# Kernel optimization log

Measured on AMD Instinct MI355X. Metric: run time of the kernel, lower is better.

The kernel has to match this reference:

```python
import jax, jax.numpy as jnp
import numpy as np

N = 50000      # nodes
E = 800000     # edges per relation
R = 2          # relations
L = 2          # conv layers
D = 128        # hidden / input channels
G = 64         # graphs in batch
C = 8          # num_classes


def setup_inputs() -> dict:
    key = jax.random.key(0)
    ks = jax.random.split(key, 6)
    x = jax.random.normal(ks[0], (N, D), dtype=jnp.float32)
    W = jax.random.normal(ks[1], (L, R, D, D), dtype=jnp.float32) * 0.05
    b = jnp.zeros((L, R, D), dtype=jnp.float32)
    lin_w = jax.random.normal(ks[2], (D, C), dtype=jnp.float32) * 0.05
    lin_b = jnp.zeros((C,), dtype=jnp.float32)
    edge_index = jax.random.randint(ks[3], (R, 2, E), 0, N, dtype=jnp.int32)
    batch = jnp.sort(jax.random.randint(ks[4], (N,), 0, G, dtype=jnp.int32))
    return {"x": x, "W": W, "b": b, "lin_w": lin_w, "lin_b": lin_b,
            "edge_index": edge_index, "batch": batch}


def _gcn_conv(x, src, dst, inv_sqrt_deg, W_r, b_r):
    """PyG GCNConv: symmetric-normalized aggregation with self loops.
    out[i] = sum_{j->i} d_i^-1/2 d_j^-1/2 (x_j W) + d_i^-1 (x_i W) + b
    where d includes the self loop (in-degree + 1)."""
    xw = x @ W_r                                   # [N, D]
    norm = inv_sqrt_deg[src] * inv_sqrt_deg[dst]   # [E]
    agg = jax.ops.segment_sum(xw[src] * norm[:, None], dst, num_segments=N)
    agg = agg + xw * (inv_sqrt_deg * inv_sqrt_deg)[:, None]  # self-loop msg
    return agg + b_r


def reference(x, W, b, lin_w, lin_b, edge_index, batch):
    # Pre-compute per-relation symmetric normalization (same for all layers).
    inv_sqrt_degs = []
    for r in range(R):
        dst = edge_index[r, 1]
        deg = jax.ops.segment_sum(jnp.ones((E,), x.dtype), dst, num_segments=N) + 1.0
        inv_sqrt_degs.append(jax.lax.rsqrt(deg))

    h = x
    for l in range(L):
        out = jnp.zeros((N, D), x.dtype)
        for r in range(R):  # HeteroConv aggr='sum' over relations
            out = out + _gcn_conv(h, edge_index[r, 0], edge_index[r, 1],
                                  inv_sqrt_degs[r], W[l, r], b[l, r])
        h = jax.nn.relu(out) if l < L - 1 else out

    # global_mean_pool over batch ids
    counts = jax.ops.segment_sum(jnp.ones((N,), x.dtype), batch, num_segments=G)
    sums = jax.ops.segment_sum(h, batch, num_segments=G)
    pooled = sums / jnp.maximum(counts, 1.0)[:, None]   # [G, D]
    # dropout(p=0.5) is identity in eval mode; final Linear
    return pooled @ lin_w + lin_b                        # [G, C]
```

## Files before the change

### kernel.cpp

```cpp
#include <hip/hip_runtime.h>
#include <math.h>

#define NN 50000
#define EE 800000
#define RR 2
#define LL 2
#define DD 128
#define GG 64
#define CCLS 8
#define NBUK 196
#define BCAP 6144
#define BCI2 14080

typedef unsigned int uint;
typedef unsigned short ushort;
typedef short bf16x8 __attribute__((ext_vector_type(8)));
typedef float f32x4 __attribute__((ext_vector_type(4)));
typedef float f32x2 __attribute__((ext_vector_type(2)));

#define OFF_H1    ((size_t)0)
#define OFF_WBT   ((size_t)12800000)
#define OFF_ISD   ((size_t)12931072)
#define OFF_RP    ((size_t)13331072)
#define OFF_CI    ((size_t)13732480)
#define OFF_ZERO  ((size_t)24771200)
#define OFF_BD    ((size_t)24805824)
#define OFF_XW    ((size_t)24805824)
#define ZO_GCUR 0
#define ZO_SUM  1600
#define ZO_CNT  34368
#define ZERO_BYTES 34624

static __device__ __forceinline__ ushort f2b(float f) {
  uint u = __float_as_uint(f);
  uint r = (u + 0x7fffu + ((u >> 16) & 1u)) >> 16;
  return (ushort)r;
}
static __device__ __forceinline__ float blo(uint u) { return __uint_as_float(u << 16); }
static __device__ __forceinline__ float bhi(uint u) { return __uint_as_float(u & 0xffff0000u); }

__global__ __launch_bounds__(256) void k_wprep(const float* __restrict__ W,
                                               ushort* __restrict__ WT) {
  int idx = blockIdx.x * 256 + threadIdx.x;
  int lr = idx >> 14;
  int rem = idx & 16383;
  int n = rem >> 7, k = rem & 127;
  WT[lr * 16384 + n * 128 + k] = f2b(W[lr * 16384 + k * 128 + n]);
}

__global__ __launch_bounds__(256) void k_part(const int* __restrict__ EI,
                                              int* __restrict__ gcur,
                                              uint* __restrict__ bdata) {
  __shared__ int hist[256];
  __shared__ int sbase[256];
  __shared__ int gbase[256];
  __shared__ int lcur[256];
  __shared__ uint stage[4096];
  __shared__ unsigned char bstage[4096];
  const int r = blockIdx.y;
  const int t = threadIdx.x;
  const int e0 = blockIdx.x * 4096;
  const int cnt = min(4096, EE - e0);
  hist[t] = 0;
  lcur[t] = 0;
  __syncthreads();

  int src[16], dst[16];
  bool val[4];
#pragma unroll
  for (int j = 0; j < 4; ++j) {
    int i4 = (j * 256 + t) * 4;
    val[j] = (i4 < cnt);
    if (val[j]) {
      int4 s4 = *(const int4*)(EI + (size_t)r * 2 * EE + e0 + i4);
      int4 d4 = *(const int4*)(EI + (size_t)r * 2 * EE + EE + e0 + i4);
      src[j * 4 + 0] = s4.x; src[j * 4 + 1] = s4.y; src[j * 4 + 2] = s4.z; src[j * 4 + 3] = s4.w;
      dst[j * 4 + 0] = d4.x; dst[j * 4 + 1] = d4.y; dst[j * 4 + 2] = d4.z; dst[j * 4 + 3] = d4.w;
#pragma unroll
      for (int i = 0; i < 4; ++i) atomicAdd(&hist[dst[j * 4 + i] >> 8], 1);
    }
  }
  __syncthreads();
  int hv = hist[t];
  if (t < NBUK && hv > 0)
    gbase[t] = atomicAdd(&gcur[r * NBUK + t], hv);
  else
    gbase[t] = 0;
  sbase[t] = hv;
  __syncthreads();
  for (int off = 1; off < 256; off <<= 1) {
    int u = (t >= off) ? sbase[t - off] : 0;
    __syncthreads();
    sbase[t] += u;
    __syncthreads();
  }
  int incl = sbase[t];
  hist[t] = incl - hv;
  __syncthreads();
#pragma unroll
  for (int j = 0; j < 4; ++j) {
    if (val[j]) {
#pragma unroll
      for (int i = 0; i < 4; ++i) {
        int d = dst[j * 4 + i];
        int b = d >> 8;
        int p = atomicAdd(&lcur[b], 1);
        int pos = hist[b] + p;
        stage[pos] = ((uint)src[j * 4 + i] << 8) | (uint)(d & 255);
        bstage[pos] = (unsigned char)b;
      }
    }
  }
  __syncthreads();
  for (int s = t; s < cnt; s += 256) {
    int b = (int)bstage[s];
    bdata[(size_t)(r * NBUK + b) * BCAP + gbase[b] + (s - hist[b])] = stage[s];
  }
}

__global__ __launch_bounds__(256) void k_csr(const uint* __restrict__ bdata,
                                             const int* __restrict__ gcur,
                                             float* __restrict__ isd,
                                             int* __restrict__ rps,
                                             int* __restrict__ rpc,
                                             int* __restrict__ ci) {
  __shared__ int lcnt0[256], lcnt1[256], lrp[256], lex[256], lend0[256];
  __shared__ int lcurA[256], lcurB[256];
  __shared__ int cstage[BCI2];
  __shared__ int shtot;
  const int b = blockIdx.x;
  const int t = threadIdx.x;
  const int cnt0 = gcur[b];
  const int cnt1 = gcur[NBUK + b];
  const uint* bd0 = bdata + (size_t)b * BCAP;
  const uint* bd1 = bdata + (size_t)(NBUK + b) * BCAP;
  lcnt0[t] = 0; lcnt1[t] = 0; lcurA[t] = 0; lcurB[t] = 0;
  __syncthreads();
  for (int s = t; s < cnt0; s += 256) atomicAdd(&lcnt0[bd0[s] & 255u], 1);
  for (int s = t; s < cnt1; s += 256) atomicAdd(&lcnt1[bd1[s] & 255u], 1);
  __syncthreads();
  const int deg0 = lcnt0[t];
  const int deg1 = lcnt1[t];
  const int node = b * 256 + t;
  const int valid = (node < NN) ? 1 : 0;
  const int nreal = deg0 + deg1 + 2;
  const int ng = valid ? ((nreal + 7) >> 3) : 0;
  const int sz = ng << 3;
  const int end0 = deg0 + 1;
  lrp[t] = sz;
  __syncthreads();
  for (int off = 1; off < 256; off <<= 1) {
    int u = (t >= off) ? lrp[t - off] : 0;
    __syncthreads();
    lrp[t] += u;
    __syncthreads();
  }
  const int incl = lrp[t];
  if (t == 255) shtot = incl;
  const int ex = incl - sz;
  lex[t] = ex;
  lend0[t] = end0;
  __syncthreads();
  const int btot = shtot;
  if (t < 32) cstage[btot + t] = NN;
  rps[node] = b * BCI2 + ex;
  rpc[node] = valid ? (ng | (end0 << 16)) : 0;
  if (valid) {
    isd[node] = rsqrtf((float)(deg0 + 1));
    isd[NN + node] = rsqrtf((float)(deg1 + 1));
    cstage[ex + deg0] = node;
    cstage[ex + end0 + deg1] = (NN + 1) + node;
    for (int p = end0 + deg1 + 1; p < sz; ++p) cstage[ex + p] = NN;
  }
  for (int s = t; s < cnt0; s += 256) {
    uint pr = bd0[s];
    int j = (int)(pr & 255u);
    int p = atomicAdd(&lcurA[j], 1);
    cstage[lex[j] + p] = (int)(pr >> 8);
  }
  for (int s = t; s < cnt1; s += 256) {
    uint pr = bd1[s];
    int j = (int)(pr & 255u);
    int p = atomicAdd(&lcurB[j], 1);
    cstage[lex[j] + lend0[j] + p] = (int)(pr >> 8) + (NN + 1);
  }
  __syncthreads();
  const int on = btot + 32;
  int* co = ci + (size_t)b * BCI2;
  for (int s = t; s < on; s += 256) co[s] = cstage[s];
}

#define AL_S 72
#define WT_S 136
template <int IN_BF16>
__global__ __launch_bounds__(256) void k_gemm(const void* __restrict__ Xv,
                                              const ushort* __restrict__ WTg,
                                              const float* __restrict__ isd,
                                              uint* __restrict__ Y) {
  __shared__ ushort WTl[128 * WT_S];
  __shared__ ushort Al[128 * AL_S];
  const int r = blockIdx.y;
  const int m0b = blockIdx.x * 128;
  const int t = threadIdx.x;
  const int w = t >> 6, L = t & 63, q = L >> 4, ln = L & 15;
  uint* Yr = Y + (size_t)r * (NN + 1) * 32;
  const ushort* WTr = WTg + (size_t)r * 16384;

#pragma unroll
  for (int i = 0; i < 8; ++i) {
    int g = t + i * 256;
    int n = g >> 4, k0 = (g & 15) * 8;
    *(uint4*)(&WTl[n * WT_S + k0]) = *(const uint4*)(WTr + n * 128 + k0);
  }

  f32x4 acc[2][8];
#pragma unroll
  for (int mt = 0; mt < 2; ++mt)
#pragma unroll
    for (int nt = 0; nt < 8; ++nt) {
      acc[mt][nt][0] = 0.f; acc[mt][nt][1] = 0.f;
      acc[mt][nt][2] = 0.f; acc[mt][nt][3] = 0.f;
    }

  for (int hh = 0; hh < 2; ++hh) {
    __syncthreads();
    {
      int row = t >> 1, ch = t & 1;
      int gm = m0b + row;
      ushort* dst = &Al[row * AL_S + ch * 32];
      if (gm < NN) {
        if (IN_BF16) {
          const uint4* xp = (const uint4*)((const ushort*)Xv + (size_t)gm * 128 + hh * 64 + ch * 32);
#pragma unroll
          for (int j = 0; j < 4; ++j) ((uint4*)dst)[j] = xp[j];
        } else {
          const float4* xp = (const float4*)((const float*)Xv + (size_t)gm * 128 + hh * 64 + ch * 32);
          ushort tmp[32];
#pragma unroll
          for (int j = 0; j < 8; ++j) {
            float4 v = xp[j];
            tmp[j * 4 + 0] = f2b(v.x); tmp[j * 4 + 1] = f2b(v.y);
            tmp[j * 4 + 2] = f2b(v.z); tmp[j * 4 + 3] = f2b(v.w);
          }
#pragma unroll
          for (int j = 0; j < 4; ++j) ((uint4*)dst)[j] = ((uint4*)tmp)[j];
        }
      } else {
        uint4 z = make_uint4(0, 0, 0, 0);
#pragma unroll
        for (int j = 0; j < 4; ++j) ((uint4*)dst)[j] = z;
      }
    }
    __syncthreads();
#pragma unroll
    for (int kk = 0; kk < 2; ++kk) {
      bf16x8 b0 = *(const bf16x8*)(&Al[(w * 32 + ln) * AL_S + kk * 32 + q * 8]);
      bf16x8 b1 = *(const bf16x8*)(&Al[(w * 32 + 16 + ln) * AL_S + kk * 32 + q * 8]);
#pragma unroll
      for (int nt = 0; nt < 8; ++nt) {
        bf16x8 a = *(const bf16x8*)(&WTl[(nt * 16 + ln) * WT_S + hh * 64 + kk * 32 + q * 8]);
        acc[0][nt] = __builtin_amdgcn_mfma_f32_16x16x32_bf16(a, b0, acc[0][nt], 0, 0, 0);
        acc[1][nt] = __builtin_amdgcn_mfma_f32_16x16x32_bf16(a, b1, acc[1][nt], 0, 0, 0);
      }
    }
  }
#pragma unroll
  for (int mt = 0; mt < 2; ++mt) {
    int m = m0b + w * 32 + mt * 16 + ln;
    if (m <= NN) {
      float sc = (m < NN) ? isd[r * NN + m] : 0.f;
      uint* yp = Yr + (size_t)m * 32;
#pragma unroll
      for (int nt = 0; nt < 8; ++nt) {
        f32x4 v = acc[mt][nt];
        uint u = __builtin_amdgcn_cvt_pk_fp8_f32(v[0] * sc, v[1] * sc, 0u, false);
        u = __builtin_amdgcn_cvt_pk_fp8_f32(v[2] * sc, v[3] * sc, u, true);
        yp[nt * 4 + q] = u;
      }
    }
  }
}

__global__ __launch_bounds__(256, 6) void k_agg(const char* __restrict__ xw,
                                                const int* __restrict__ rps,
                                                const int* __restrict__ rpc,
                                                const int* __restrict__ ci,
                                                const float* __restrict__ isd,
                                                const float* __restrict__ bias,
                                                uint* __restrict__ hout, int relu_flag) {
  const int w = threadIdx.x >> 6;
  const int lane = threadIdx.x & 63;
  const int g = lane >> 3, c = lane & 7;
  const int node = blockIdx.x * 4 + w;
  const size_t cb = (size_t)c * 16;

  const int meta = rpc[node];
  const int ng = meta & 0xffff;
  const int end0 = (meta >> 16) & 0xffff;
  const int lim = ng << 3;
  const int* ce = ci + rps[node];
  const float di0 = isd[node < NN ? node : 0];
  const float di1 = isd[NN + (node < NN ? node : 0)];

  int ip = g;
  int s0 = ce[ip]; s0 = (ip < lim) ? s0 : NN; ip += 8;
  uint4 d0 = *(const uint4*)(xw + (((size_t)(uint)s0 << 7) + cb));
  int s1 = ce[ip]; s1 = (ip < lim) ? s1 : NN; ip += 8;
  uint4 d1 = *(const uint4*)(xw + (((size_t)(uint)s1 << 7) + cb));
  int s2 = ce[ip]; s2 = (ip < lim) ? s2 : NN; ip += 8;
  uint4 d2 = *(const uint4*)(xw + (((size_t)(uint)s2 << 7) + cb));

  f32x2 acc[8];
#pragma unroll
  for (int j = 0; j < 8; ++j) { acc[j][0] = 0.f; acc[j][1] = 0.f; }

  int slotc = g;
  for (int q = 0; q < ng; ++q) {
    int s3 = ce[ip]; s3 = (ip < lim) ? s3 : NN; ip += 8;
    uint4 d3 = *(const uint4*)(xw + (((size_t)(uint)s3 << 7) + cb));
    const float sc = (slotc < end0) ? di0 : di1;
    slotc += 8;
    f32x2 sc2; sc2[0] = sc; sc2[1] = sc;
    f32x2 v;
    v = __builtin_amdgcn_cvt_pk_f32_fp8(d0.x, false); acc[0] += v * sc2;
    v = __builtin_amdgcn_cvt_pk_f32_fp8(d0.x, true);  acc[1] += v * sc2;
    v = __builtin_amdgcn_cvt_pk_f32_fp8(d0.y, false); acc[2] += v * sc2;
    v = __builtin_amdgcn_cvt_pk_f32_fp8(d0.y, true);  acc[3] += v * sc2;
    v = __builtin_amdgcn_cvt_pk_f32_fp8(d0.z, false); acc[4] += v * sc2;
    v = __builtin_amdgcn_cvt_pk_f32_fp8(d0.z, true);  acc[5] += v * sc2;
    v = __builtin_amdgcn_cvt_pk_f32_fp8(d0.w, false); acc[6] += v * sc2;
    v = __builtin_amdgcn_cvt_pk_f32_fp8(d0.w, true);  acc[7] += v * sc2;
    d0 = d1; d1 = d2; d2 = d3;
  }

#pragma unroll
  for (int mask = 8; mask <= 32; mask <<= 1) {
#pragma unroll
    for (int j = 0; j < 8; ++j) {
      f32x2 o;
      o[0] = __shfl_xor(acc[j][0], mask);
      o[1] = __shfl_xor(acc[j][1], mask);
      acc[j] += o;
    }
  }

  if (g == 0 && node < NN) {
    const float4* p0 = (const float4*)(bias + c * 16);
    const float4* p1 = (const float4*)(bias + DD + c * 16);
    float o[16];
#pragma unroll
    for (int j = 0; j < 4; ++j) {
      float4 a = p0[j], bq = p1[j];
      o[4 * j + 0] = acc[2 * j][0] + a.x + bq.x;
      o[4 * j + 1] = acc[2 * j][1] + a.y + bq.y;
      o[4 * j + 2] = acc[2 * j + 1][0] + a.z + bq.z;
      o[4 * j + 3] = acc[2 * j + 1][1] + a.w + bq.w;
    }
    if (relu_flag) {
#pragma unroll
      for (int j = 0; j < 16; ++j) o[j] = fmaxf(o[j], 0.f);
    }
    uint pk[8];
#pragma unroll
    for (int j = 0; j < 8; ++j)
      pk[j] = (uint)f2b(o[2 * j]) | ((uint)f2b(o[2 * j + 1]) << 16);
    uint4* dst = (uint4*)(hout + (size_t)node * 64) + c * 2;
    dst[0] = make_uint4(pk[0], pk[1], pk[2], pk[3]);
    dst[1] = make_uint4(pk[4], pk[5], pk[6], pk[7]);
  }
}

#define PCHUNK 32
__global__ __launch_bounds__(64) void k_pool(const uint* __restrict__ h,
                                             const int* __restrict__ batch,
                                             float* __restrict__ sums,
                                             int* __restrict__ counts) {
  int lane = threadIdx.x;
  int n0 = blockIdx.x * PCHUNK;
  int n1 = n0 + PCHUNK;
  if (n1 > NN) n1 = NN;
  if (n0 >= NN) return;
  float aLo = 0.f, aHi = 0.f;
  int cnt = 0;
  int g = batch[n0];
  uint u = h[(size_t)n0 * 64 + lane];
  for (int n = n0; n < n1; ++n) {
    uint unext = 0;
    int gnext = g;
    if (n + 1 < n1) {
      unext = h[(size_t)(n + 1) * 64 + lane];
      gnext = batch[n + 1];
    }
    aLo += blo(u);
    aHi += bhi(u);
    cnt++;
    if (n + 1 < n1 && gnext != g) {
      atomicAdd(&sums[g * DD + lane * 2], aLo);
      atomicAdd(&sums[g * DD + lane * 2 + 1], aHi);
      if (lane == 0) atomicAdd(&counts[g], cnt);
      aLo = 0.f; aHi = 0.f; cnt = 0;
      g = gnext;
    }
    u = unext;
  }
  atomicAdd(&sums[g * DD + lane * 2], aLo);
  atomicAdd(&sums[g * DD + lane * 2 + 1], aHi);
  if (lane == 0) atomicAdd(&counts[g], cnt);
}

__global__ __launch_bounds__(512) void k_final(const float* __restrict__ sums,
                                               const int* __restrict__ counts,
                                               const float* __restrict__ lin_w,
                                               const float* __restrict__ lin_b,
                                               float* __restrict__ out) {
  int t = threadIdx.x;
  int g = t >> 3, co = t & 7;
  float cnt = (float)counts[g];
  if (cnt < 1.f) cnt = 1.f;
  float inv = 1.f / cnt;
  float v = lin_b[co];
  for (int d = 0; d < DD; ++d) v += (sums[g * DD + d] * inv) * lin_w[d * CCLS + co];
  out[t] = v;
}

extern "C" void kernel_launch(void* const* d_in, const int* in_sizes, int n_in,
                              void* d_out, int out_size, void* d_ws, size_t ws_size,
                              hipStream_t stream) {
  (void)in_sizes; (void)n_in; (void)out_size; (void)ws_size;
  const float* x     = (const float*)d_in[0];
  const float* W     = (const float*)d_in[1];
  const float* b     = (const float*)d_in[2];
  const float* lin_w = (const float*)d_in[3];
  const float* lin_b = (const float*)d_in[4];
  const int*   EI    = (const int*)d_in[5];
  const int*   batch = (const int*)d_in[6];
  float* out = (float*)d_out;

  char* ws = (char*)d_ws;
  uint*   h1    = (uint*)(ws + OFF_H1);
  ushort* WbfT  = (ushort*)(ws + OFF_WBT);
  float*  isd   = (float*)(ws + OFF_ISD);
  int*    rps   = (int*)(ws + OFF_RP);
  int*    rpc   = rps + NBUK * 256;
  int*    ci    = (int*)(ws + OFF_CI);
  uint*   bdata = (uint*)(ws + OFF_BD);
  uint*   xw    = (uint*)(ws + OFF_XW);
  char*   zb    = ws + OFF_ZERO;
  int*    gcur  = (int*)(zb + ZO_GCUR);
  float*  sums  = (float*)(zb + ZO_SUM);
  int*    counts= (int*)(zb + ZO_CNT);

  (void)hipMemsetAsync(zb, 0, ZERO_BYTES, stream);

  k_wprep<<<256, 256, 0, stream>>>(W, WbfT);
  k_part<<<dim3((EE + 4095) / 4096, RR), 256, 0, stream>>>(EI, gcur, bdata);
  k_csr<<<NBUK, 256, 0, stream>>>(bdata, gcur, isd, rps, rpc, ci);

  for (int l = 0; l < LL; ++l) {
    const ushort* WTl_g = WbfT + (size_t)l * RR * DD * DD;
    if (l == 0)
      k_gemm<0><<<dim3((NN + 127) / 128, RR), 256, 0, stream>>>((const void*)x, WTl_g, isd, xw);
    else
      k_gemm<1><<<dim3((NN + 127) / 128, RR), 256, 0, stream>>>((const void*)h1, WTl_g, isd, xw);
    k_agg<<<(NBUK * 256) / 4, 256, 0, stream>>>((const char*)xw, rps, rpc, ci, isd,
                                                b + (size_t)l * RR * DD, h1,
                                                (l < LL - 1) ? 1 : 0);
  }
  k_pool<<<(NN + PCHUNK - 1) / PCHUNK, 64, 0, stream>>>(h1, batch, sums, counts);
  k_final<<<1, GG * CCLS, 0, stream>>>(sums, counts, lin_w, lin_b, out);
}
```

Measured before the change: 272.7 us.

## Split aggregation into column slices with 16 edge slots per node

The aggregation kernel now handles two nodes per wavefront with 16 edge slots each. Each lane loads 16 bytes of a 32-byte column slice, and four blocks cover the four slices of the same node group. CSR padding changes to multiples of 16 so more neighbor gathers are in flight per node. The deep three-stage prefetch becomes a single-stage one, and occupancy bounds are raised. The costs are that the CSR edge lists are re-read once per slice, low-degree nodes carry more padding, and a wave's two nodes both loop to the larger group count.

```diff
diff --git a/kernel.cpp b/kernel.cpp
--- a/kernel.cpp
+++ b/kernel.cpp
@@ -144,8 +144,8 @@
   const int node = b * 256 + t;
   const int valid = (node < NN) ? 1 : 0;
   const int nreal = deg0 + deg1 + 2;
-  const int ng = valid ? ((nreal + 7) >> 3) : 0;
-  const int sz = ng << 3;
+  const int ng = valid ? ((nreal + 15) >> 4) : 0;
+  const int sz = ng << 4;
   const int end0 = deg0 + 1;
   lrp[t] = sz;
   __syncthreads();
@@ -281,7 +281,7 @@
   }
 }
 
-__global__ __launch_bounds__(256, 6) void k_agg(const char* __restrict__ xw,
+__global__ __launch_bounds__(256, 8) void k_agg(const char* __restrict__ xw,
                                                 const int* __restrict__ rps,
                                                 const int* __restrict__ rpc,
                                                 const int* __restrict__ ci,
@@ -290,36 +290,44 @@
                                                 uint* __restrict__ hout, int relu_flag) {
   const int w = threadIdx.x >> 6;
   const int lane = threadIdx.x & 63;
-  const int g = lane >> 3, c = lane & 7;
-  const int node = blockIdx.x * 4 + w;
-  const size_t cb = (size_t)c * 16;
+  const int sub = lane >> 5;
+  const int slot = (lane >> 1) & 15;
+  const int half = lane & 1;
+  const int slice = blockIdx.x & 3;
+  const int grp = blockIdx.x >> 2;
+  const int node = grp * 8 + w * 2 + sub;
+  const int nsafe = (node < NN) ? node : 0;
 
   const int meta = rpc[node];
   const int ng = meta & 0xffff;
   const int end0 = (meta >> 16) & 0xffff;
-  const int lim = ng << 3;
+  const int lim = ng << 4;
   const int* ce = ci + rps[node];
-  const float di0 = isd[node < NN ? node : 0];
-  const float di1 = isd[NN + (node < NN ? node : 0)];
-
-  int ip = g;
-  int s0 = ce[ip]; s0 = (ip < lim) ? s0 : NN; ip += 8;
-  uint4 d0 = *(const uint4*)(xw + (((size_t)(uint)s0 << 7) + cb));
-  int s1 = ce[ip]; s1 = (ip < lim) ? s1 : NN; ip += 8;
-  uint4 d1 = *(const uint4*)(xw + (((size_t)(uint)s1 << 7) + cb));
-  int s2 = ce[ip]; s2 = (ip < lim) ? s2 : NN; ip += 8;
-  uint4 d2 = *(const uint4*)(xw + (((size_t)(uint)s2 << 7) + cb));
+  const float di0 = isd[nsafe];
+  const float di1 = isd[NN + nsafe];
+  const char* xs = xw + (size_t)slice * 32 + (size_t)half * 16;
+
+  int ot = __shfl_xor(ng, 32);
+  const int mng = (ng > ot) ? ng : ot;
+
+  int pos = slot;
+  int tl = ce[pos];
+  int s0 = (pos < lim) ? tl : NN;
+  uint4 d0 = *(const uint4*)(xs + ((size_t)(uint)s0 << 7));
+  pos += 16;
 
   f32x2 acc[8];
 #pragma unroll
   for (int j = 0; j < 8; ++j) { acc[j][0] = 0.f; acc[j][1] = 0.f; }
 
-  int slotc = g;
-  for (int q = 0; q < ng; ++q) {
-    int s3 = ce[ip]; s3 = (ip < lim) ? s3 : NN; ip += 8;
-    uint4 d3 = *(const uint4*)(xw + (((size_t)(uint)s3 << 7) + cb));
-    const float sc = (slotc < end0) ? di0 : di1;
-    slotc += 8;
+  int spos = slot;
+  for (int q = 0; q < mng; ++q) {
+    int tn = ce[pos];
+    int s1 = (pos < lim) ? tn : NN;
+    pos += 16;
+    uint4 d1 = *(const uint4*)(xs + ((size_t)(uint)s1 << 7));
+    const float sc = (spos < end0) ? di0 : di1;
+    spos += 16;
     f32x2 sc2; sc2[0] = sc; sc2[1] = sc;
     f32x2 v;
     v = __builtin_amdgcn_cvt_pk_f32_fp8(d0.x, false); acc[0] += v * sc2;
@@ -330,11 +338,11 @@
     v = __builtin_amdgcn_cvt_pk_f32_fp8(d0.z, true);  acc[5] += v * sc2;
     v = __builtin_amdgcn_cvt_pk_f32_fp8(d0.w, false); acc[6] += v * sc2;
     v = __builtin_amdgcn_cvt_pk_f32_fp8(d0.w, true);  acc[7] += v * sc2;
-    d0 = d1; d1 = d2; d2 = d3;
-  }
-
-#pragma unroll
-  for (int mask = 8; mask <= 32; mask <<= 1) {
+    d0 = d1;
+  }
+
+#pragma unroll
+  for (int mask = 2; mask <= 16; mask <<= 1) {
 #pragma unroll
     for (int j = 0; j < 8; ++j) {
       f32x2 o;
@@ -344,9 +352,10 @@
     }
   }
 
-  if (g == 0 && node < NN) {
-    const float4* p0 = (const float4*)(bias + c * 16);
-    const float4* p1 = (const float4*)(bias + DD + c * 16);
+  if ((lane & 30) == 0 && node < NN) {
+    const int ch0 = slice * 32 + half * 16;
+    const float4* p0 = (const float4*)(bias + ch0);
+    const float4* p1 = (const float4*)(bias + DD + ch0);
     float o[16];
 #pragma unroll
     for (int j = 0; j < 4; ++j) {
@@ -364,7 +373,7 @@
 #pragma unroll
     for (int j = 0; j < 8; ++j)
       pk[j] = (uint)f2b(o[2 * j]) | ((uint)f2b(o[2 * j + 1]) << 16);
-    uint4* dst = (uint4*)(hout + (size_t)node * 64) + c * 2;
+    uint4* dst = (uint4*)(hout + (size_t)node * 64 + slice * 16 + half * 8);
     dst[0] = make_uint4(pk[0], pk[1], pk[2], pk[3]);
     dst[1] = make_uint4(pk[4], pk[5], pk[6], pk[7]);
   }
@@ -462,9 +471,9 @@
       k_gemm<0><<<dim3((NN + 127) / 128, RR), 256, 0, stream>>>((const void*)x, WTl_g, isd, xw);
     else
       k_gemm<1><<<dim3((NN + 127) / 128, RR), 256, 0, stream>>>((const void*)h1, WTl_g, isd, xw);
-    k_agg<<<(NBUK * 256) / 4, 256, 0, stream>>>((const char*)xw, rps, rpc, ci, isd,
-                                                b + (size_t)l * RR * DD, h1,
-                                                (l < LL - 1) ? 1 : 0);
+    k_agg<<<4 * (NBUK * 256 / 8), 256, 0, stream>>>((const char*)xw, rps, rpc, ci, isd,
+                                                    b + (size_t)l * RR * DD, h1,
+                                                    (l < LL - 1) ? 1 : 0);
   }
   k_pool<<<(NN + PCHUNK - 1) / PCHUNK, 64, 0, stream>>>(h1, batch, sums, counts);
   k_final<<<1, GG * CCLS, 0, stream>>>(sums, counts, lin_w, lin_b, out);
```

Result: slower. 368.3 us (+35.0%).

## Reorder GCN to aggregate-then-transform with fused per-relation concatenated GEMM

Applied to the files above, without the earlier changes.

Each layer now aggregates fp8 features per relation first, using separate accumulators. It writes both relation sums as one bf16 row of width 256, then runs a single K=256 GEMM against both relations' concatenated weights, with bias and ReLU fused in. The per-edge source normalization is packed as bf16 into the CSR entries next to a 16-bit source index, and the CSR build is split into two kernels. Input x is quantized to fp8 once up front. This removes one GEMM launch per layer and the per-slot relation selects, but adds a wider intermediate write and read and fp8 precision on raw inputs.

```diff
diff --git a/kernel.cpp b/kernel.cpp
--- a/kernel.cpp
+++ b/kernel.cpp
@@ -9,8 +9,8 @@
 #define GG 64
 #define CCLS 8
 #define NBUK 196
-#define BCAP 6144
-#define BCI2 14080
+#define BCAP 4608
+#define BCI  12000
 
 typedef unsigned int uint;
 typedef unsigned short ushort;
@@ -18,14 +18,13 @@
 typedef float f32x4 __attribute__((ext_vector_type(4)));
 typedef float f32x2 __attribute__((ext_vector_type(2)));
 
-#define OFF_H1    ((size_t)0)
-#define OFF_WBT   ((size_t)12800000)
-#define OFF_ISD   ((size_t)12931072)
-#define OFF_RP    ((size_t)13331072)
-#define OFF_CI    ((size_t)13732480)
-#define OFF_ZERO  ((size_t)24771200)
-#define OFF_BD    ((size_t)24805824)
-#define OFF_XW    ((size_t)24805824)
+#define OFF_AGG   ((size_t)0)
+#define OFF_WBT   ((size_t)25600000)
+#define OFF_ISD   ((size_t)25731072)
+#define OFF_RP    ((size_t)26131072)
+#define OFF_CI    ((size_t)26733184)
+#define OFF_ZERO  ((size_t)36141184)
+#define OFF_T     ((size_t)36175808)
 #define ZO_GCUR 0
 #define ZO_SUM  1600
 #define ZO_CNT  34368
@@ -43,9 +42,24 @@
                                                ushort* __restrict__ WT) {
   int idx = blockIdx.x * 256 + threadIdx.x;
   int lr = idx >> 14;
+  int l = lr >> 1, r = lr & 1;
   int rem = idx & 16383;
   int n = rem >> 7, k = rem & 127;
-  WT[lr * 16384 + n * 128 + k] = f2b(W[lr * 16384 + k * 128 + n]);
+  WT[l * 32768 + n * 256 + r * 128 + k] = f2b(W[lr * 16384 + k * 128 + n]);
+}
+
+__global__ __launch_bounds__(256) void k_xq(const float* __restrict__ x,
+                                            uint* __restrict__ T) {
+  int idx = blockIdx.x * 256 + threadIdx.x;
+  if (idx >= (NN + 1) * 32) return;
+  int row = idx >> 5, q = idx & 31;
+  uint u = 0;
+  if (row < NN) {
+    float4 a = ((const float4*)x)[(size_t)row * 32 + q];
+    u = __builtin_amdgcn_cvt_pk_fp8_f32(a.x, a.y, 0u, false);
+    u = __builtin_amdgcn_cvt_pk_fp8_f32(a.z, a.w, u, true);
+  }
+  T[idx] = u;
 }
 
 __global__ __launch_bounds__(256) void k_part(const int* __restrict__ EI,
@@ -118,23 +132,20 @@
   }
 }
 
-__global__ __launch_bounds__(256) void k_csr(const uint* __restrict__ bdata,
-                                             const int* __restrict__ gcur,
-                                             float* __restrict__ isd,
-                                             int* __restrict__ rps,
-                                             int* __restrict__ rpc,
-                                             int* __restrict__ ci) {
-  __shared__ int lcnt0[256], lcnt1[256], lrp[256], lex[256], lend0[256];
-  __shared__ int lcurA[256], lcurB[256];
-  __shared__ int cstage[BCI2];
-  __shared__ int shtot;
+__global__ __launch_bounds__(256) void k_csr1(const uint* __restrict__ bdata,
+                                              const int* __restrict__ gcur,
+                                              float* __restrict__ isd,
+                                              int* __restrict__ rps,
+                                              int* __restrict__ rpc,
+                                              int* __restrict__ degs) {
+  __shared__ int lcnt0[256], lcnt1[256], lrp[256];
   const int b = blockIdx.x;
   const int t = threadIdx.x;
   const int cnt0 = gcur[b];
   const int cnt1 = gcur[NBUK + b];
   const uint* bd0 = bdata + (size_t)b * BCAP;
   const uint* bd1 = bdata + (size_t)(NBUK + b) * BCAP;
-  lcnt0[t] = 0; lcnt1[t] = 0; lcurA[t] = 0; lcurB[t] = 0;
+  lcnt0[t] = 0; lcnt1[t] = 0;
   __syncthreads();
   for (int s = t; s < cnt0; s += 256) atomicAdd(&lcnt0[bd0[s] & 255u], 1);
   for (int s = t; s < cnt1; s += 256) atomicAdd(&lcnt1[bd1[s] & 255u], 1);
@@ -143,10 +154,9 @@
   const int deg1 = lcnt1[t];
   const int node = b * 256 + t;
   const int valid = (node < NN) ? 1 : 0;
-  const int nreal = deg0 + deg1 + 2;
-  const int ng = valid ? ((nreal + 7) >> 3) : 0;
-  const int sz = ng << 3;
-  const int end0 = deg0 + 1;
+  const int ng0 = valid ? ((deg0 + 8) >> 3) : 0;
+  const int ng1 = valid ? ((deg1 + 8) >> 3) : 0;
+  const int sz = (ng0 + ng1) << 3;
   lrp[t] = sz;
   __syncthreads();
   for (int off = 1; off < 256; off <<= 1) {
@@ -155,139 +165,99 @@
     lrp[t] += u;
     __syncthreads();
   }
-  const int incl = lrp[t];
-  if (t == 255) shtot = incl;
-  const int ex = incl - sz;
-  lex[t] = ex;
-  lend0[t] = end0;
-  __syncthreads();
-  const int btot = shtot;
-  if (t < 32) cstage[btot + t] = NN;
-  rps[node] = b * BCI2 + ex;
-  rpc[node] = valid ? (ng | (end0 << 16)) : 0;
+  const int ex = lrp[t] - sz;
+  rps[node] = b * BCI + ex;
+  rpc[node] = ng0 | (ng1 << 16);
+  degs[node] = deg0 | (deg1 << 16);
   if (valid) {
     isd[node] = rsqrtf((float)(deg0 + 1));
     isd[NN + node] = rsqrtf((float)(deg1 + 1));
-    cstage[ex + deg0] = node;
-    cstage[ex + end0 + deg1] = (NN + 1) + node;
-    for (int p = end0 + deg1 + 1; p < sz; ++p) cstage[ex + p] = NN;
+  }
+}
+
+__global__ __launch_bounds__(256) void k_csr2(const uint* __restrict__ bdata,
+                                              const int* __restrict__ gcur,
+                                              const float* __restrict__ isd,
+                                              const int* __restrict__ rps,
+                                              const int* __restrict__ rpc,
+                                              const int* __restrict__ degs,
+                                              int* __restrict__ ci) {
+  __shared__ int lex[256], lb1[256], lcurA[256], lcurB[256];
+  __shared__ int cstage[BCI];
+  __shared__ int shtot;
+  const int b = blockIdx.x;
+  const int t = threadIdx.x;
+  const int node = b * 256 + t;
+  const int cnt0 = gcur[b];
+  const int cnt1 = gcur[NBUK + b];
+  const uint* bd0 = bdata + (size_t)b * BCAP;
+  const uint* bd1 = bdata + (size_t)(NBUK + b) * BCAP;
+  const int ex = rps[node] - b * BCI;
+  const int meta = rpc[node];
+  const int ng0 = meta & 0xffff, ng1 = (meta >> 16) & 0xffff;
+  const int dg = degs[node];
+  const int deg0 = dg & 0xffff, deg1 = (dg >> 16) & 0xffff;
+  lex[t] = ex;
+  lb1[t] = ng0 << 3;
+  lcurA[t] = 0;
+  lcurB[t] = 0;
+  if (t == 255) shtot = ex + ((ng0 + ng1) << 3);
+  __syncthreads();
+  const int tot = shtot;
+  if (t < 32) cstage[tot + t] = NN;
+  if (node < NN) {
+    cstage[ex + deg0] = node | ((uint)f2b(isd[node]) << 16);
+    for (int p = deg0 + 1; p < (ng0 << 3); ++p) cstage[ex + p] = NN;
+    const int e1 = ex + (ng0 << 3);
+    cstage[e1 + deg1] = node | ((uint)f2b(isd[NN + node]) << 16);
+    for (int p = deg1 + 1; p < (ng1 << 3); ++p) cstage[e1 + p] = NN;
   }
   for (int s = t; s < cnt0; s += 256) {
     uint pr = bd0[s];
     int j = (int)(pr & 255u);
+    int sr = (int)(pr >> 8);
     int p = atomicAdd(&lcurA[j], 1);
-    cstage[lex[j] + p] = (int)(pr >> 8);
+    cstage[lex[j] + p] = sr | ((uint)f2b(isd[sr]) << 16);
   }
   for (int s = t; s < cnt1; s += 256) {
     uint pr = bd1[s];
     int j = (int)(pr & 255u);
+    int sr = (int)(pr >> 8);
     int p = atomicAdd(&lcurB[j], 1);
-    cstage[lex[j] + lend0[j] + p] = (int)(pr >> 8) + (NN + 1);
-  }
-  __syncthreads();
-  const int on = btot + 32;
-  int* co = ci + (size_t)b * BCI2;
+    cstage[lex[j] + lb1[j] + p] = sr | ((uint)f2b(isd[NN + sr]) << 16);
+  }
+  __syncthreads();
+  int* co = ci + (size_t)b * BCI;
+  const int on = tot + 32;
   for (int s = t; s < on; s += 256) co[s] = cstage[s];
 }
 
-#define AL_S 72
-#define WT_S 136
-template <int IN_BF16>
-__global__ __launch_bounds__(256) void k_gemm(const void* __restrict__ Xv,
-                                              const ushort* __restrict__ WTg,
-                                              const float* __restrict__ isd,
-                                              uint* __restrict__ Y) {
-  __shared__ ushort WTl[128 * WT_S];
-  __shared__ ushort Al[128 * AL_S];
-  const int r = blockIdx.y;
-  const int m0b = blockIdx.x * 128;
-  const int t = threadIdx.x;
-  const int w = t >> 6, L = t & 63, q = L >> 4, ln = L & 15;
-  uint* Yr = Y + (size_t)r * (NN + 1) * 32;
-  const ushort* WTr = WTg + (size_t)r * 16384;
-
-#pragma unroll
-  for (int i = 0; i < 8; ++i) {
-    int g = t + i * 256;
-    int n = g >> 4, k0 = (g & 15) * 8;
-    *(uint4*)(&WTl[n * WT_S + k0]) = *(const uint4*)(WTr + n * 128 + k0);
-  }
-
-  f32x4 acc[2][8];
-#pragma unroll
-  for (int mt = 0; mt < 2; ++mt)
-#pragma unroll
-    for (int nt = 0; nt < 8; ++nt) {
-      acc[mt][nt][0] = 0.f; acc[mt][nt][1] = 0.f;
-      acc[mt][nt][2] = 0.f; acc[mt][nt][3] = 0.f;
-    }
-
-  for (int hh = 0; hh < 2; ++hh) {
-    __syncthreads();
-    {
-      int row = t >> 1, ch = t & 1;
-      int gm = m0b + row;
-      ushort* dst = &Al[row * AL_S + ch * 32];
-      if (gm < NN) {
-        if (IN_BF16) {
-          const uint4* xp = (const uint4*)((const ushort*)Xv + (size_t)gm * 128 + hh * 64 + ch * 32);
-#pragma unroll
-          for (int j = 0; j < 4; ++j) ((uint4*)dst)[j] = xp[j];
-        } else {
-          const float4* xp = (const float4*)((const float*)Xv + (size_t)gm * 128 + hh * 64 + ch * 32);
-          ushort tmp[32];
-#pragma unroll
-          for (int j = 0; j < 8; ++j) {
-            float4 v = xp[j];
-            tmp[j * 4 + 0] = f2b(v.x); tmp[j * 4 + 1] = f2b(v.y);
-            tmp[j * 4 + 2] = f2b(v.z); tmp[j * 4 + 3] = f2b(v.w);
-          }
-#pragma unroll
-          for (int j = 0; j < 4; ++j) ((uint4*)dst)[j] = ((uint4*)tmp)[j];
-        }
-      } else {
-        uint4 z = make_uint4(0, 0, 0, 0);
-#pragma unroll
-        for (int j = 0; j < 4; ++j) ((uint4*)dst)[j] = z;
-      }
-    }
-    __syncthreads();
-#pragma unroll
-    for (int kk = 0; kk < 2; ++kk) {
-      bf16x8 b0 = *(const bf16x8*)(&Al[(w * 32 + ln) * AL_S + kk * 32 + q * 8]);
-      bf16x8 b1 = *(const bf16x8*)(&Al[(w * 32 + 16 + ln) * AL_S + kk * 32 + q * 8]);
-#pragma unroll
-      for (int nt = 0; nt < 8; ++nt) {
-        bf16x8 a = *(const bf16x8*)(&WTl[(nt * 16 + ln) * WT_S + hh * 64 + kk * 32 + q * 8]);
-        acc[0][nt] = __builtin_amdgcn_mfma_f32_16x16x32_bf16(a, b0, acc[0][nt], 0, 0, 0);
-        acc[1][nt] = __builtin_amdgcn_mfma_f32_16x16x32_bf16(a, b1, acc[1][nt], 0, 0, 0);
-      }
-    }
-  }
-#pragma unroll
-  for (int mt = 0; mt < 2; ++mt) {
-    int m = m0b + w * 32 + mt * 16 + ln;
-    if (m <= NN) {
-      float sc = (m < NN) ? isd[r * NN + m] : 0.f;
-      uint* yp = Yr + (size_t)m * 32;
-#pragma unroll
-      for (int nt = 0; nt < 8; ++nt) {
-        f32x4 v = acc[mt][nt];
-        uint u = __builtin_amdgcn_cvt_pk_fp8_f32(v[0] * sc, v[1] * sc, 0u, false);
-        u = __builtin_amdgcn_cvt_pk_fp8_f32(v[2] * sc, v[3] * sc, u, true);
-        yp[nt * 4 + q] = u;
-      }
-    }
-  }
-}
-
-__global__ __launch_bounds__(256, 6) void k_agg(const char* __restrict__ xw,
+#define AGG_STEP(A)                                                            \
+  {                                                                            \
+    uint e2 = (uint)ce[ip];                                                    \
+    int s2 = (ip < lim) ? (int)(e2 & 0xffffu) : NN;                            \
+    float f2 = bhi(e2);                                                        \
+    ip += 8;                                                                   \
+    uint4 d2 = *(const uint4*)(Tb + ((((size_t)(uint)s2) << 7) + cb));         \
+    f32x2 sc; sc[0] = f0; sc[1] = f0;                                          \
+    f32x2 v;                                                                   \
+    v = __builtin_amdgcn_cvt_pk_f32_fp8(d0.x, false); A[0] += v * sc;          \
+    v = __builtin_amdgcn_cvt_pk_f32_fp8(d0.x, true);  A[1] += v * sc;          \
+    v = __builtin_amdgcn_cvt_pk_f32_fp8(d0.y, false); A[2] += v * sc;          \
+    v = __builtin_amdgcn_cvt_pk_f32_fp8(d0.y, true);  A[3] += v * sc;          \
+    v = __builtin_amdgcn_cvt_pk_f32_fp8(d0.z, false); A[4] += v * sc;          \
+    v = __builtin_amdgcn_cvt_pk_f32_fp8(d0.z, true);  A[5] += v * sc;          \
+    v = __builtin_amdgcn_cvt_pk_f32_fp8(d0.w, false); A[6] += v * sc;          \
+    v = __builtin_amdgcn_cvt_pk_f32_fp8(d0.w, true);  A[7] += v * sc;          \
+    d0 = d1; d1 = d2; f0 = f1; f1 = f2;                                        \
+  }
+
+__global__ __launch_bounds__(256, 6) void k_agg(const char* __restrict__ Tb,
                                                 const int* __restrict__ rps,
                                                 const int* __restrict__ rpc,
                                                 const int* __restrict__ ci,
                                                 const float* __restrict__ isd,
-                                                const float* __restrict__ bias,
-                                                uint* __restrict__ hout, int relu_flag) {
+                                                ushort* __restrict__ aggo) {
   const int w = threadIdx.x >> 6;
   const int lane = threadIdx.x & 63;
   const int g = lane >> 3, c = lane & 7;
@@ -295,78 +265,159 @@
   const size_t cb = (size_t)c * 16;
 
   const int meta = rpc[node];
-  const int ng = meta & 0xffff;
-  const int end0 = (meta >> 16) & 0xffff;
-  const int lim = ng << 3;
+  const int ng0 = meta & 0xffff;
+  const int ng1 = (meta >> 16) & 0xffff;
+  const int lim = (ng0 + ng1) << 3;
   const int* ce = ci + rps[node];
-  const float di0 = isd[node < NN ? node : 0];
-  const float di1 = isd[NN + (node < NN ? node : 0)];
+  const int nsafe = (node < NN) ? node : 0;
+  const float di0 = isd[nsafe];
+  const float di1 = isd[NN + nsafe];
 
   int ip = g;
-  int s0 = ce[ip]; s0 = (ip < lim) ? s0 : NN; ip += 8;
-  uint4 d0 = *(const uint4*)(xw + (((size_t)(uint)s0 << 7) + cb));
-  int s1 = ce[ip]; s1 = (ip < lim) ? s1 : NN; ip += 8;
-  uint4 d1 = *(const uint4*)(xw + (((size_t)(uint)s1 << 7) + cb));
-  int s2 = ce[ip]; s2 = (ip < lim) ? s2 : NN; ip += 8;
-  uint4 d2 = *(const uint4*)(xw + (((size_t)(uint)s2 << 7) + cb));
-
-  f32x2 acc[8];
-#pragma unroll
-  for (int j = 0; j < 8; ++j) { acc[j][0] = 0.f; acc[j][1] = 0.f; }
-
-  int slotc = g;
-  for (int q = 0; q < ng; ++q) {
-    int s3 = ce[ip]; s3 = (ip < lim) ? s3 : NN; ip += 8;
-    uint4 d3 = *(const uint4*)(xw + (((size_t)(uint)s3 << 7) + cb));
-    const float sc = (slotc < end0) ? di0 : di1;
-    slotc += 8;
-    f32x2 sc2; sc2[0] = sc; sc2[1] = sc;
-    f32x2 v;
-    v = __builtin_amdgcn_cvt_pk_f32_fp8(d0.x, false); acc[0] += v * sc2;
-    v = __builtin_amdgcn_cvt_pk_f32_fp8(d0.x, true);  acc[1] += v * sc2;
-    v = __builtin_amdgcn_cvt_pk_f32_fp8(d0.y, false); acc[2] += v * sc2;
-    v = __builtin_amdgcn_cvt_pk_f32_fp8(d0.y, true);  acc[3] += v * sc2;
-    v = __builtin_amdgcn_cvt_pk_f32_fp8(d0.z, false); acc[4] += v * sc2;
-    v = __builtin_amdgcn_cvt_pk_f32_fp8(d0.z, true);  acc[5] += v * sc2;
-    v = __builtin_amdgcn_cvt_pk_f32_fp8(d0.w, false); acc[6] += v * sc2;
-    v = __builtin_amdgcn_cvt_pk_f32_fp8(d0.w, true);  acc[7] += v * sc2;
-    d0 = d1; d1 = d2; d2 = d3;
-  }
+  uint e0 = (uint)ce[ip];
+  int s0 = (ip < lim) ? (int)(e0 & 0xffffu) : NN;
+  float f0 = bhi(e0);
+  ip += 8;
+  uint4 d0 = *(const uint4*)(Tb + ((((size_t)(uint)s0) << 7) + cb));
+  uint e1 = (uint)ce[ip];
+  int s1 = (ip < lim) ? (int)(e1 & 0xffffu) : NN;
+  float f1 = bhi(e1);
+  ip += 8;
+  uint4 d1 = *(const uint4*)(Tb + ((((size_t)(uint)s1) << 7) + cb));
+
+  f32x2 a0[8], a1[8];
+#pragma unroll
+  for (int j = 0; j < 8; ++j) { a0[j][0] = 0.f; a0[j][1] = 0.f; a1[j][0] = 0.f; a1[j][1] = 0.f; }
+
+  for (int q = 0; q < ng0; ++q) AGG_STEP(a0);
+  for (int q = 0; q < ng1; ++q) AGG_STEP(a1);
 
 #pragma unroll
   for (int mask = 8; mask <= 32; mask <<= 1) {
 #pragma unroll
     for (int j = 0; j < 8; ++j) {
-      f32x2 o;
-      o[0] = __shfl_xor(acc[j][0], mask);
-      o[1] = __shfl_xor(acc[j][1], mask);
-      acc[j] += o;
+      f32x2 o, p;
+      o[0] = __shfl_xor(a0[j][0], mask);
+      o[1] = __shfl_xor(a0[j][1], mask);
+      p[0] = __shfl_xor(a1[j][0], mask);
+      p[1] = __shfl_xor(a1[j][1], mask);
+      a0[j] += o;
+      a1[j] += p;
     }
   }
 
   if (g == 0 && node < NN) {
-    const float4* p0 = (const float4*)(bias + c * 16);
-    const float4* p1 = (const float4*)(bias + DD + c * 16);
-    float o[16];
+    ushort* row = aggo + (size_t)node * 256;
+    uint pk[8];
 #pragma unroll
     for (int j = 0; j < 4; ++j) {
-      float4 a = p0[j], bq = p1[j];
-      o[4 * j + 0] = acc[2 * j][0] + a.x + bq.x;
-      o[4 * j + 1] = acc[2 * j][1] + a.y + bq.y;
-      o[4 * j + 2] = acc[2 * j + 1][0] + a.z + bq.z;
-      o[4 * j + 3] = acc[2 * j + 1][1] + a.w + bq.w;
-    }
-    if (relu_flag) {
-#pragma unroll
-      for (int j = 0; j < 16; ++j) o[j] = fmaxf(o[j], 0.f);
-    }
-    uint pk[8];
-#pragma unroll
-    for (int j = 0; j < 8; ++j)
-      pk[j] = (uint)f2b(o[2 * j]) | ((uint)f2b(o[2 * j + 1]) << 16);
-    uint4* dst = (uint4*)(hout + (size_t)node * 64) + c * 2;
-    dst[0] = make_uint4(pk[0], pk[1], pk[2], pk[3]);
-    dst[1] = make_uint4(pk[4], pk[5], pk[6], pk[7]);
+      pk[2 * j] = (uint)f2b(a0[2 * j][0] * di0) | ((uint)f2b(a0[2 * j][1] * di0) << 16);
+      pk[2 * j + 1] = (uint)f2b(a0[2 * j + 1][0] * di0) | ((uint)f2b(a0[2 * j + 1][1] * di0) << 16);
+    }
+    *(uint4*)(row + c * 16) = make_uint4(pk[0], pk[1], pk[2], pk[3]);
+    *(uint4*)(row + c * 16 + 8) = make_uint4(pk[4], pk[5], pk[6], pk[7]);
+#pragma unroll
+    for (int j = 0; j < 4; ++j) {
+      pk[2 * j] = (uint)f2b(a1[2 * j][0] * di1) | ((uint)f2b(a1[2 * j][1] * di1) << 16);
+      pk[2 * j + 1] = (uint)f2b(a1[2 * j + 1][0] * di1) | ((uint)f2b(a1[2 * j + 1][1] * di1) << 16);
+    }
+    *(uint4*)(row + 128 + c * 16) = make_uint4(pk[0], pk[1], pk[2], pk[3]);
+    *(uint4*)(row + 128 + c * 16 + 8) = make_uint4(pk[4], pk[5], pk[6], pk[7]);
+  }
+}
+
+#define AL_S 72
+#define WT_S 72
+template <int OUT>
+__global__ __launch_bounds__(256) void k_gemm(const ushort* __restrict__ A,
+                                              const ushort* __restrict__ WTg,
+                                              const float* __restrict__ bias,
+                                              uint* __restrict__ Yfp8,
+                                              ushort* __restrict__ Ybf) {
+  __shared__ ushort WTl[128 * WT_S];
+  __shared__ ushort Al[64 * AL_S];
+  const int m0b = blockIdx.x * 64;
+  const int t = threadIdx.x;
+  const int w = t >> 6, L = t & 63, q = L >> 4, ln = L & 15;
+
+  f32x4 acc[8];
+#pragma unroll
+  for (int nt = 0; nt < 8; ++nt) {
+    acc[nt][0] = 0.f; acc[nt][1] = 0.f; acc[nt][2] = 0.f; acc[nt][3] = 0.f;
+  }
+
+  for (int hh = 0; hh < 4; ++hh) {
+    __syncthreads();
+    {
+      int n = t >> 1, half = t & 1;
+#pragma unroll
+      for (int j = 0; j < 4; ++j)
+        *(uint4*)(&WTl[n * WT_S + half * 32 + j * 8]) =
+            *(const uint4*)(WTg + n * 256 + hh * 64 + half * 32 + j * 8);
+      int row = t >> 2, seg = t & 3;
+      int gm = m0b + row;
+      if (gm < NN) {
+#pragma unroll
+        for (int j = 0; j < 2; ++j)
+          *(uint4*)(&Al[row * AL_S + seg * 16 + j * 8]) =
+              *(const uint4*)(A + (size_t)gm * 256 + hh * 64 + seg * 16 + j * 8);
+      } else {
+        uint4 z = make_uint4(0, 0, 0, 0);
+#pragma unroll
+        for (int j = 0; j < 2; ++j) *(uint4*)(&Al[row * AL_S + seg * 16 + j * 8]) = z;
+      }
+    }
+    __syncthreads();
+#pragma unroll
+    for (int kk = 0; kk < 2; ++kk) {
+      bf16x8 bfr = *(const bf16x8*)(&Al[(w * 16 + ln) * AL_S + kk * 32 + q * 8]);
+#pragma unroll
+      for (int nt = 0; nt < 8; ++nt) {
+        bf16x8 a = *(const bf16x8*)(&WTl[(nt * 16 + ln) * WT_S + kk * 32 + q * 8]);
+        acc[nt] = __builtin_amdgcn_mfma_f32_16x16x32_bf16(a, bfr, acc[nt], 0, 0, 0);
+      }
+    }
+  }
+  const int m = m0b + w * 16 + ln;
+  if (OUT == 0) {
+    if (m < NN) {
+      uint* yp = Yfp8 + (size_t)m * 32;
+#pragma unroll
+      for (int nt = 0; nt < 8; ++nt) {
+        int n0 = nt * 16 + q * 4;
+        float4 bL = *(const float4*)(bias + n0);
+        float4 bH = *(const float4*)(bias + 128 + n0);
+        f32x4 v = acc[nt];
+        float o0 = fmaxf(v[0] + bL.x + bH.x, 0.f);
+        float o1 = fmaxf(v[1] + bL.y + bH.y, 0.f);
+        float o2 = fmaxf(v[2] + bL.z + bH.z, 0.f);
+        float o3 = fmaxf(v[3] + bL.w + bH.w, 0.f);
+        uint u = __builtin_amdgcn_cvt_pk_fp8_f32(o0, o1, 0u, false);
+        u = __builtin_amdgcn_cvt_pk_fp8_f32(o2, o3, u, true);
+        yp[nt * 4 + q] = u;
+      }
+    } else if (m == NN) {
+      uint* yp = Yfp8 + (size_t)m * 32;
+#pragma unroll
+      for (int nt = 0; nt < 8; ++nt) yp[nt * 4 + q] = 0u;
+    }
+  } else {
+    if (m < NN) {
+      uint* yp = (uint*)(Ybf + (size_t)m * 256);
+#pragma unroll
+      for (int nt = 0; nt < 8; ++nt) {
+        int n0 = nt * 16 + q * 4;
+        float4 bL = *(const float4*)(bias + n0);
+        float4 bH = *(const float4*)(bias + 128 + n0);
+        f32x4 v = acc[nt];
+        float o0 = v[0] + bL.x + bH.x;
+        float o1 = v[1] + bL.y + bH.y;
+        float o2 = v[2] + bL.z + bH.z;
+        float o3 = v[3] + bL.w + bH.w;
+        yp[nt * 8 + q * 2] = (uint)f2b(o0) | ((uint)f2b(o1) << 16);
+        yp[nt * 8 + q * 2 + 1] = (uint)f2b(o2) | ((uint)f2b(o3) << 16);
+      }
+    }
   }
 }
 
@@ -383,12 +434,12 @@
   float aLo = 0.f, aHi = 0.f;
   int cnt = 0;
   int g = batch[n0];
-  uint u = h[(size_t)n0 * 64 + lane];
+  uint u = h[(size_t)n0 * 128 + lane];
   for (int n = n0; n < n1; ++n) {
     uint unext = 0;
     int gnext = g;
     if (n + 1 < n1) {
-      unext = h[(size_t)(n + 1) * 64 + lane];
+      unext = h[(size_t)(n + 1) * 128 + lane];
       gnext = batch[n + 1];
     }
     aLo += blo(u);
@@ -437,14 +488,15 @@
   float* out = (float*)d_out;
 
   char* ws = (char*)d_ws;
-  uint*   h1    = (uint*)(ws + OFF_H1);
-  ushort* WbfT  = (ushort*)(ws + OFF_WBT);
+  ushort* agg   = (ushort*)(ws + OFF_AGG);
+  uint*   bdata = (uint*)(ws + OFF_AGG);
+  ushort* Ws    = (ushort*)(ws + OFF_WBT);
   float*  isd   = (float*)(ws + OFF_ISD);
   int*    rps   = (int*)(ws + OFF_RP);
   int*    rpc   = rps + NBUK * 256;
+  int*    degs  = rpc + NBUK * 256;
   int*    ci    = (int*)(ws + OFF_CI);
-  uint*   bdata = (uint*)(ws + OFF_BD);
-  uint*   xw    = (uint*)(ws + OFF_XW);
+  uint*   T     = (uint*)(ws + OFF_T);
   char*   zb    = ws + OFF_ZERO;
   int*    gcur  = (int*)(zb + ZO_GCUR);
   float*  sums  = (float*)(zb + ZO_SUM);
@@ -452,20 +504,19 @@
 
   (void)hipMemsetAsync(zb, 0, ZERO_BYTES, stream);
 
-  k_wprep<<<256, 256, 0, stream>>>(W, WbfT);
+  k_wprep<<<256, 256, 0, stream>>>(W, Ws);
+  k_xq<<<((NN + 1) * 32 + 255) / 256, 256, 0, stream>>>(x, T);
   k_part<<<dim3((EE + 4095) / 4096, RR), 256, 0, stream>>>(EI, gcur, bdata);
-  k_csr<<<NBUK, 256, 0, stream>>>(bdata, gcur, isd, rps, rpc, ci);
-
-  for (int l = 0; l < LL; ++l) {
-    const ushort* WTl_g = WbfT + (size_t)l * RR * DD * DD;
-    if (l == 0)
-      k_gemm<0><<<dim3((NN + 127) / 128, RR), 256, 0, stream>>>((const void*)x, WTl_g, isd, xw);
-    else
-      k_gemm<1><<<dim3((NN + 127) / 128, RR), 256, 0, stream>>>((const void*)h1, WTl_g, isd, xw);
-    k_agg<<<(NBUK * 256) / 4, 256, 0, stream>>>((const char*)xw, rps, rpc, ci, isd,
-                                                b + (size_t)l * RR * DD, h1,
-                                                (l < LL - 1) ? 1 : 0);
-  }
-  k_pool<<<(NN + PCHUNK - 1) / PCHUNK, 64, 0, stream>>>(h1, batch, sums, counts);
+  k_csr1<<<NBUK, 256, 0, stream>>>(bdata, gcur, isd, rps, rpc, degs);
+  k_csr2<<<NBUK, 256, 0, stream>>>(bdata, gcur, isd, rps, rpc, degs, ci);
+
+  const int gagg = NBUK * 256 / 4;
+  const int ggemm = (NN + 63) / 64;
+  k_agg<<<gagg, 256, 0, stream>>>((const char*)T, rps, rpc, ci, isd, agg);
+  k_gemm<0><<<ggemm, 256, 0, stream>>>(agg, Ws, b, T, nullptr);
+  k_agg<<<gagg, 256, 0, stream>>>((const char*)T, rps, rpc, ci, isd, agg);
+  k_gemm<1><<<ggemm, 256, 0, stream>>>(agg, Ws + 32768, b + 256, nullptr, agg);
+
+  k_pool<<<(NN + PCHUNK - 1) / PCHUNK, 64, 0, stream>>>((const uint*)agg, batch, sums, counts);
   k_final<<<1, GG * CCLS, 0, stream>>>(sums, counts, lin_w, lin_b, out);
 }
```

Measured after the change: 297.5 us. 1.09x slower.
